# Performance work log

Measured on AMD Instinct MI355X. Metric: run time of the kernel, lower is better.

Reference implementation:

```python
import jax, jax.numpy as jnp
import numpy as np

N_NODES = 50000
N_EDGES = 800000
IN_DIM = 256
HID_DIM = 256
BATCH = 1


def setup_inputs() -> dict:
    key = jax.random.key(0)
    k1, k2, k3, k4, k5, k6, k7 = jax.random.split(key, 7)
    x = jax.random.normal(k1, (BATCH, N_NODES, IN_DIM), dtype=jnp.float32)
    edge_index = jax.random.randint(k2, (2, N_EDGES), 0, N_NODES, dtype=jnp.int32)
    # GCNConv params (glorot-ish scale)
    W1 = jax.random.normal(k3, (IN_DIM, HID_DIM), dtype=jnp.float32) * (1.0 / np.sqrt(IN_DIM))
    b1 = jnp.zeros((HID_DIM,), dtype=jnp.float32)
    W2 = jax.random.normal(k4, (HID_DIM, IN_DIM), dtype=jnp.float32) * (1.0 / np.sqrt(HID_DIM))
    b2 = jnp.zeros((IN_DIM,), dtype=jnp.float32)
    return {"x": x, "edge_index": edge_index, "W1": W1, "b1": b1, "W2": W2, "b2": b2}


def _gcn_conv(x, src, dst, norm, W, b):
    # x: [B, N, F_in] -> [B, N, F_out]; src/dst/norm: [E + N] (self-loops appended)
    h = x @ W                                   # linear transform first (PyG GCNConv)
    msg = h[:, src, :] * norm[None, :, None]    # gather + degree normalization
    out = jnp.zeros(h.shape, h.dtype).at[:, dst, :].add(msg)  # scatter-add
    return out + b


def _gcn_norm(edge_index, num_nodes):
    # symmetric normalization with self-loops: 1/sqrt(deg_i * deg_j)
    loop = jnp.arange(num_nodes, dtype=edge_index.dtype)
    src = jnp.concatenate([edge_index[0], loop])
    dst = jnp.concatenate([edge_index[1], loop])
    deg = jax.ops.segment_sum(jnp.ones(dst.shape, jnp.float32), dst, num_segments=num_nodes)
    dinv = jnp.where(deg > 0, jax.lax.rsqrt(jnp.maximum(deg, 1.0)), 0.0)
    norm = dinv[src] * dinv[dst]
    return src, dst, norm


def reference(x, edge_index, W1, b1, W2, b2):
    src, dst, norm = _gcn_norm(edge_index, x.shape[1])
    h = jax.nn.relu(_gcn_conv(x, src, dst, norm, W1, b1))
    h = jax.nn.relu(_gcn_conv(h, src, dst, norm, W2, b2))
    return (x + h) * 0.5
```

## Files before the change

kernel.cpp:

```cpp
#include <hip/hip_runtime.h>
#include <stdint.h>

#define NN 50000
#define NPAD 50048
#define NE 800000
#define DIM 256
#define NCHUNK 8
#define ZROW NN
#define GLC 64

typedef __attribute__((ext_vector_type(8))) short short8;
typedef __attribute__((ext_vector_type(4))) unsigned short ushort4v;
typedef __attribute__((ext_vector_type(8))) unsigned short ushort8v;
typedef __attribute__((ext_vector_type(4))) float floatx4;
typedef __attribute__((ext_vector_type(2))) float float2v;
typedef __attribute__((ext_vector_type(4))) uint32_t uint4v;
typedef __attribute__((ext_vector_type(4))) int int4v;

__device__ __forceinline__ uint16_t f2bf(float f) {
  union { float f; uint32_t u; } v; v.f = f;
  uint32_t r = v.u + 0x7fffu + ((v.u >> 16) & 1u);
  return (uint16_t)(r >> 16);
}
__device__ __forceinline__ float bf2f(uint16_t h) {
  union { uint32_t u; float f; } v; v.u = ((uint32_t)h) << 16;
  return v.f;
}

__device__ __forceinline__ void pkacc(float2v& a, uint32_t u) {
  union { uint32_t u; float f; } lo, hi;
  lo.u = u << 16;
  hi.u = u & 0xffff0000u;
  float2v val;
  val[0] = lo.f;
  val[1] = hi.f;
  asm("v_pk_add_f32 %0, %1, %0" : "+v"(a) : "v"(val));
}

__device__ __forceinline__ void stage16(const uint16_t* gp, short* lbase, int lane) {
#if __has_builtin(__builtin_amdgcn_global_load_lds)
  __builtin_amdgcn_global_load_lds((__attribute__((address_space(1))) void*)gp,
                                   (__attribute__((address_space(3))) void*)lbase,
                                   16, 0, 0);
#else
  *(ushort8v*)((uint16_t*)lbase + lane * 8) = *(const ushort8v*)gp;
#endif
}

__global__ __launch_bounds__(256) void k_init(int* __restrict__ fill, uint16_t* __restrict__ g,
                                              int* __restrict__ gl,
                                              const float* __restrict__ W1,
                                              const float* __restrict__ W2,
                                              uint16_t* __restrict__ Wt1,
                                              uint16_t* __restrict__ Wt2) {
  __shared__ float t[32][33];
  if (blockIdx.x >= 3125) {
    int bid = blockIdx.x - 3125;
    const float* W = (bid < 64) ? W1 : W2;
    uint16_t* Wt = (bid < 64) ? Wt1 : Wt2;
    bid &= 63;
    int bx = bid & 7, by = bid >> 3;
    int tx = threadIdx.x & 31, ty = threadIdx.x >> 5;
#pragma unroll
    for (int q = 0; q < 4; ++q)
      t[ty + q * 8][tx] = W[(size_t)(by * 32 + ty + q * 8) * 256 + bx * 32 + tx];
    __syncthreads();
#pragma unroll
    for (int q = 0; q < 4; ++q)
      Wt[(size_t)(bx * 32 + ty + q * 8) * 256 + by * 32 + tx] = f2bf(t[tx][ty + q * 8]);
    return;
  }
  int i4 = blockIdx.x * 256 + threadIdx.x;
  int4v z4 = {ZROW, ZROW, ZROW, ZROW};
  ((int4v*)gl)[i4] = z4;
  if (i4 < NPAD / 4) {
    int4v zz = {0, 0, 0, 0};
    ((int4v*)fill)[i4] = zz;
  }
  if (blockIdx.x < NCHUNK) {
    uint32_t* q = (uint32_t*)(g + ((size_t)blockIdx.x * NPAD + NN) * 32);
    for (int k = threadIdx.x; k < 768; k += 256) q[k] = 0;
  }
}

__global__ __launch_bounds__(256) void k_fill(const int* __restrict__ src,
                                              const int* __restrict__ dst,
                                              int* __restrict__ fill,
                                              int* __restrict__ gl) {
  int e = blockIdx.x * 256 + threadIdx.x;
  if (e < NE) {
    int d = dst[e];
    int old = atomicAdd(&fill[d], 1);
    if (old < GLC - 1) gl[d * GLC + old] = src[e];
  }
}

__global__ __launch_bounds__(256) void k_deg(const int* __restrict__ fill,
                                             int* __restrict__ gl) {
  int i = blockIdx.x * 256 + threadIdx.x;
  if (i < NN) {
    int deg = fill[i];
    if (deg < GLC) gl[i * GLC + deg] = i;
  }
}

#define BM 128
#define BK 32

template <int SPLIT>
__global__ __launch_bounds__(256) void k_gemm(const uint16_t* __restrict__ Ab,
                                              const float* __restrict__ Af,
                                              const uint16_t* __restrict__ Wt,
                                              const int* __restrict__ degp,
                                              uint16_t* __restrict__ C, int M) {
  __shared__ short Ash[2][BM * BK];
  __shared__ short Asl[2][BM * BK];
  __shared__ short Bs[2][128 * BK];

  const int tid = threadIdx.x;
  const int wave = tid >> 6, lane = tid & 63;
  const int wm = wave >> 1, wn = wave & 1;
  const int m16 = lane & 15, q = lane >> 4;
  const int rowBase = blockIdx.x * BM;
  const int colBase = blockIdx.y * 128;
  const int rsub = lane >> 2;
  const int kch = (lane & 3) * 8;

  auto stageB = [&](int kc, int buf) {
#pragma unroll
    for (int p2 = 0; p2 < 2; ++p2) {
      int n = p2 * 64 + wave * 16 + rsub;
      stage16(Wt + (size_t)(colBase + n) * 256 + kc * 32 + kch,
              &Bs[buf][(p2 * 64 + wave * 16) * BK], lane);
    }
  };
  auto stageA = [&](int kc, int buf) {
#pragma unroll
    for (int p2 = 0; p2 < 2; ++p2) {
      int r = rowBase + p2 * 64 + wave * 16 + rsub;
      stage16(Ab + ((size_t)kc * NPAD + r) * 32 + kch,
              &Ash[buf][(p2 * 64 + wave * 16) * BK], lane);
    }
  };
  auto loadA = [&](int kc, float4* f) {
#pragma unroll
    for (int p2 = 0; p2 < 2; ++p2) {
      int r = rowBase + p2 * 64 + wave * 16 + rsub;
      int rs = r < NN ? r : NN - 1;
      const float* xp = Af + (size_t)rs * DIM + kc * 32 + kch;
      f[2 * p2] = *(const float4*)xp;
      f[2 * p2 + 1] = *(const float4*)(xp + 4);
    }
  };
  auto writeA = [&](int buf, const float4* f) {
#pragma unroll
    for (int p2 = 0; p2 < 2; ++p2) {
      float ff[8] = {f[2 * p2].x, f[2 * p2].y, f[2 * p2].z, f[2 * p2].w,
                     f[2 * p2 + 1].x, f[2 * p2 + 1].y, f[2 * p2 + 1].z, f[2 * p2 + 1].w};
      short8 h8, l8;
#pragma unroll
      for (int u = 0; u < 8; ++u) {
        uint16_t hh = f2bf(ff[u]);
        h8[u] = (short)hh;
        l8[u] = (short)f2bf(ff[u] - bf2f(hh));
      }
      *(short8*)&Ash[buf][(p2 * 64 + wave * 16 + rsub) * BK + kch] = h8;
      *(short8*)&Asl[buf][(p2 * 64 + wave * 16 + rsub) * BK + kch] = l8;
    }
  };

  floatx4 acc[4][4];
#pragma unroll
  for (int i = 0; i < 4; ++i)
#pragma unroll
    for (int j = 0; j < 4; ++j) acc[i][j] = (floatx4)(0.0f);

  if (SPLIT) {
    float4 f[4];
    loadA(0, f);
    writeA(0, f);
  } else {
    stageA(0, 0);
  }
  stageB(0, 0);
  __syncthreads();

  for (int kc = 0; kc < 8; ++kc) {
    const int cur = kc & 1, nxt = cur ^ 1;
    float4 g4[4];
    if (kc < 7) {
      if (SPLIT) loadA(kc + 1, g4);
      else stageA(kc + 1, nxt);
      stageB(kc + 1, nxt);
    }

    short8 ah[4], al[4], b[4];
#pragma unroll
    for (int i = 0; i < 4; ++i) {
      int r = wm * 64 + i * 16 + m16;
      ah[i] = *(const short8*)(&Ash[cur][r * BK + q * 8]);
      if (SPLIT) al[i] = *(const short8*)(&Asl[cur][r * BK + q * 8]);
    }
#pragma unroll
    for (int j = 0; j < 4; ++j) {
      int n = wn * 64 + j * 16 + m16;
      b[j] = *(const short8*)(&Bs[cur][n * BK + q * 8]);
    }
#pragma unroll
    for (int i = 0; i < 4; ++i)
#pragma unroll
      for (int j = 0; j < 4; ++j) {
        if (SPLIT)
          acc[i][j] = __builtin_amdgcn_mfma_f32_16x16x32_bf16(al[i], b[j], acc[i][j], 0, 0, 0);
        acc[i][j] = __builtin_amdgcn_mfma_f32_16x16x32_bf16(ah[i], b[j], acc[i][j], 0, 0, 0);
      }

    if (SPLIT && kc < 7) writeA(nxt, g4);
    __syncthreads();
  }

#pragma unroll
  for (int i = 0; i < 4; ++i) {
#pragma unroll
    for (int reg = 0; reg < 4; ++reg) {
      int row = rowBase + wm * 64 + i * 16 + q * 4 + reg;
      if (row < M) {
        float dv = rsqrtf((float)(degp[row] + 1));
#pragma unroll
        for (int j = 0; j < 4; ++j) {
          int col = colBase + wn * 64 + j * 16 + m16;
          C[((size_t)(col >> 5) * NPAD + row) * 32 + (col & 31)] = f2bf(acc[i][j][reg] * dv);
        }
      }
    }
  }
}

template <int FINAL>
__global__ __launch_bounds__(256) void k_agg(const uint16_t* __restrict__ gb,
                                             const int* __restrict__ gl,
                                             const int* __restrict__ degp,
                                             const float* __restrict__ bias,
                                             const float* __restrict__ x,
                                             uint16_t* __restrict__ outb,
                                             float* __restrict__ outf) {
  const int c = blockIdx.x & 7;
  const int dg = blockIdx.x >> 3;
  const int wave = threadIdx.x >> 6, lane = threadIdx.x & 63;
  const int dl = lane >> 4;
  const int s = (lane >> 2) & 3;
  const int fl = lane & 3;
  const int d = dg * 16 + wave * 4 + dl;
  const uint16_t* gp = gb + (size_t)c * NPAD * 32;
  const uint32_t coff = (uint32_t)fl * 8;

  int ia[6];
#pragma unroll
  for (int j = 0; j < 6; ++j) ia[j] = gl[d * GLC + s + 4 * j];
  uint4v v[6];
#pragma unroll
  for (int j = 0; j < 6; ++j)
    v[j] = *(const uint4v*)(gp + (uint32_t)ia[j] * 32u + coff);

  float2v acc2[4];
#pragma unroll
  for (int j = 0; j < 4; ++j) acc2[j] = (float2v)(0.0f);
#pragma unroll
  for (int j = 0; j < 6; ++j) {
    pkacc(acc2[0], v[j][0]);
    pkacc(acc2[1], v[j][1]);
    pkacc(acc2[2], v[j][2]);
    pkacc(acc2[3], v[j][3]);
  }

  int deg = degp[d];
  if (deg >= 24) {
    for (int e = 24 + s; e <= deg; e += 4) {
      int si = gl[d * GLC + e];
      uint4v vt = *(const uint4v*)(gp + (uint32_t)si * 32u + coff);
      pkacc(acc2[0], vt[0]); pkacc(acc2[1], vt[1]);
      pkacc(acc2[2], vt[2]); pkacc(acc2[3], vt[3]);
    }
  }

#pragma unroll
  for (int j = 0; j < 4; ++j) {
    acc2[j][0] += __shfl_xor(acc2[j][0], 4);
    acc2[j][1] += __shfl_xor(acc2[j][1], 4);
    acc2[j][0] += __shfl_xor(acc2[j][0], 8);
    acc2[j][1] += __shfl_xor(acc2[j][1], 8);
  }

  if (s == 0) {
    float dd = rsqrtf((float)(deg + 1));
    int feat = c * 32 + fl * 8;
    float4 b0 = *(const float4*)(bias + feat);
    float4 b1 = *(const float4*)(bias + feat + 4);
    float bb[8] = {b0.x, b0.y, b0.z, b0.w, b1.x, b1.y, b1.z, b1.w};
    float r[8];
#pragma unroll
    for (int j = 0; j < 4; ++j) {
      r[2 * j] = fmaxf(dd * acc2[j][0] + bb[2 * j], 0.f);
      r[2 * j + 1] = fmaxf(dd * acc2[j][1] + bb[2 * j + 1], 0.f);
    }
    if (FINAL) {
      float4 x0 = *(const float4*)(x + (size_t)d * DIM + feat);
      float4 x1 = *(const float4*)(x + (size_t)d * DIM + feat + 4);
      float xx[8] = {x0.x, x0.y, x0.z, x0.w, x1.x, x1.y, x1.z, x1.w};
      float4 o0, o1;
      o0.x = (xx[0] + r[0]) * 0.5f; o0.y = (xx[1] + r[1]) * 0.5f;
      o0.z = (xx[2] + r[2]) * 0.5f; o0.w = (xx[3] + r[3]) * 0.5f;
      o1.x = (xx[4] + r[4]) * 0.5f; o1.y = (xx[5] + r[5]) * 0.5f;
      o1.z = (xx[6] + r[6]) * 0.5f; o1.w = (xx[7] + r[7]) * 0.5f;
      *(float4*)(outf + (size_t)d * DIM + feat) = o0;
      *(float4*)(outf + (size_t)d * DIM + feat + 4) = o1;
    } else {
      ushort8v o;
#pragma unroll
      for (int t = 0; t < 8; ++t) o[t] = f2bf(r[t]);
      *(ushort8v*)(outb + ((size_t)c * NPAD + d) * 32 + fl * 8) = o;
    }
  }
}

extern "C" void kernel_launch(void* const* d_in, const int* in_sizes, int n_in,
                              void* d_out, int out_size, void* d_ws, size_t ws_size,
                              hipStream_t stream) {
  const float* x  = (const float*)d_in[0];
  const int*   ei = (const int*)d_in[1];
  const float* W1 = (const float*)d_in[2];
  const float* b1 = (const float*)d_in[3];
  const float* W2 = (const float*)d_in[4];
  const float* b2 = (const float*)d_in[5];
  float* out = (float*)d_out;

  int*      fill   = (int*)d_ws;
  int*      gl     = fill + NPAD;
  uint16_t* Wt1    = (uint16_t*)(gl + NN * GLC);
  uint16_t* Wt2    = Wt1 + 256 * 256;
  uint16_t* g      = Wt2 + 256 * 256;
  uint16_t* h1     = g + (size_t)NPAD * DIM;

  const int* esrc = ei;
  const int* edst = ei + NE;

  k_init<<<3253, 256, 0, stream>>>(fill, g, gl, W1, W2, Wt1, Wt2);
  k_fill<<<(NE + 255) / 256, 256, 0, stream>>>(esrc, edst, fill, gl);
  k_deg<<<196, 256, 0, stream>>>(fill, gl);

  const int aggBlocks = NCHUNK * (NN / 16);
  dim3 ggrid(NPAD / BM, 2);
  k_gemm<1><<<ggrid, 256, 0, stream>>>(nullptr, x, Wt1, fill, g, NN);
  k_agg<0><<<aggBlocks, 256, 0, stream>>>(g, gl, fill, b1, nullptr, h1, nullptr);
  k_gemm<0><<<ggrid, 256, 0, stream>>>(h1, nullptr, Wt2, fill, g, NN);
  k_agg<1><<<aggBlocks, 256, 0, stream>>>(g, gl, fill, b2, x, nullptr, out);
}
```

Baseline: 288.0 us.

## Use 16-bit neighbor lists and degree-sorted node order in aggregation

```diff
diff --git a/kernel.cpp b/kernel.cpp
--- a/kernel.cpp
+++ b/kernel.cpp
@@ -10,7 +10,6 @@
 #define GLC 64
 
 typedef __attribute__((ext_vector_type(8))) short short8;
-typedef __attribute__((ext_vector_type(4))) unsigned short ushort4v;
 typedef __attribute__((ext_vector_type(8))) unsigned short ushort8v;
 typedef __attribute__((ext_vector_type(4))) float floatx4;
 typedef __attribute__((ext_vector_type(2))) float float2v;
@@ -48,14 +47,15 @@
 }
 
 __global__ __launch_bounds__(256) void k_init(int* __restrict__ fill, uint16_t* __restrict__ g,
-                                              int* __restrict__ gl,
+                                              uint16_t* __restrict__ gl,
+                                              int* __restrict__ bins,
                                               const float* __restrict__ W1,
                                               const float* __restrict__ W2,
                                               uint16_t* __restrict__ Wt1,
                                               uint16_t* __restrict__ Wt2) {
   __shared__ float t[32][33];
-  if (blockIdx.x >= 3125) {
-    int bid = blockIdx.x - 3125;
+  if (blockIdx.x >= 1563) {
+    int bid = blockIdx.x - 1563;
     const float* W = (bid < 64) ? W1 : W2;
     uint16_t* Wt = (bid < 64) ? Wt1 : Wt2;
     bid &= 63;
@@ -70,12 +70,18 @@
       Wt[(size_t)(bx * 32 + ty + q * 8) * 256 + by * 32 + tx] = f2bf(t[tx][ty + q * 8]);
     return;
   }
-  int i4 = blockIdx.x * 256 + threadIdx.x;
-  int4v z4 = {ZROW, ZROW, ZROW, ZROW};
-  ((int4v*)gl)[i4] = z4;
-  if (i4 < NPAD / 4) {
+  int i = blockIdx.x * 256 + threadIdx.x;
+  if (i < 400000) {
+    ushort8v z8 = {ZROW, ZROW, ZROW, ZROW, ZROW, ZROW, ZROW, ZROW};
+    ((ushort8v*)gl)[i] = z8;
+  }
+  if (i < NPAD / 4) {
     int4v zz = {0, 0, 0, 0};
-    ((int4v*)fill)[i4] = zz;
+    ((int4v*)fill)[i] = zz;
+  }
+  if (i < 32) {
+    int4v zz = {0, 0, 0, 0};
+    ((int4v*)bins)[i] = zz;
   }
   if (blockIdx.x < NCHUNK) {
     uint32_t* q = (uint32_t*)(g + ((size_t)blockIdx.x * NPAD + NN) * 32);
@@ -86,21 +92,41 @@
 __global__ __launch_bounds__(256) void k_fill(const int* __restrict__ src,
                                               const int* __restrict__ dst,
                                               int* __restrict__ fill,
-                                              int* __restrict__ gl) {
+                                              uint16_t* __restrict__ gl) {
   int e = blockIdx.x * 256 + threadIdx.x;
   if (e < NE) {
     int d = dst[e];
     int old = atomicAdd(&fill[d], 1);
-    if (old < GLC - 1) gl[d * GLC + old] = src[e];
-  }
-}
-
-__global__ __launch_bounds__(256) void k_deg(const int* __restrict__ fill,
-                                             int* __restrict__ gl) {
+    if (old < GLC - 1) gl[d * GLC + old] = (uint16_t)src[e];
+  }
+}
+
+__global__ __launch_bounds__(256) void k_degbins(const int* __restrict__ fill,
+                                                 uint16_t* __restrict__ gl,
+                                                 int* __restrict__ bins) {
   int i = blockIdx.x * 256 + threadIdx.x;
   if (i < NN) {
     int deg = fill[i];
-    if (deg < GLC) gl[i * GLC + deg] = i;
+    if (deg < GLC) gl[i * GLC + deg] = (uint16_t)i;
+    atomicAdd(&bins[deg < 63 ? deg : 63], 1);
+  }
+}
+
+__global__ __launch_bounds__(256) void k_scatter(const int* __restrict__ fill,
+                                                 int* __restrict__ bins,
+                                                 uint16_t* __restrict__ perm) {
+  __shared__ int soff[64];
+  if (threadIdx.x == 0) {
+    int a = 0;
+    for (int k = 0; k < 64; ++k) { soff[k] = a; a += bins[k]; }
+  }
+  __syncthreads();
+  int i = blockIdx.x * 256 + threadIdx.x;
+  if (i < NN) {
+    int deg = fill[i];
+    if (deg > 63) deg = 63;
+    int pos = soff[deg] + atomicAdd(&bins[64 + deg], 1);
+    perm[pos] = (uint16_t)i;
   }
 }
 
@@ -238,7 +264,8 @@
 
 template <int FINAL>
 __global__ __launch_bounds__(256) void k_agg(const uint16_t* __restrict__ gb,
-                                             const int* __restrict__ gl,
+                                             const uint16_t* __restrict__ perm,
+                                             const uint16_t* __restrict__ gl,
                                              const int* __restrict__ degp,
                                              const float* __restrict__ bias,
                                              const float* __restrict__ x,
@@ -250,36 +277,48 @@
   const int dl = lane >> 4;
   const int s = (lane >> 2) & 3;
   const int fl = lane & 3;
-  const int d = dg * 16 + wave * 4 + dl;
+  const int d = (int)perm[dg * 16 + wave * 4 + dl];
+  const int deg = degp[d];
   const uint16_t* gp = gb + (size_t)c * NPAD * 32;
   const uint32_t coff = (uint32_t)fl * 8;
-
-  int ia[6];
-#pragma unroll
-  for (int j = 0; j < 6; ++j) ia[j] = gl[d * GLC + s + 4 * j];
-  uint4v v[6];
-#pragma unroll
-  for (int j = 0; j < 6; ++j)
-    v[j] = *(const uint4v*)(gp + (uint32_t)ia[j] * 32u + coff);
+  const uint32_t* glr = (const uint32_t*)(gl + (size_t)d * GLC);
+
+  uint32_t w0 = glr[s], w1 = glr[s + 4], w2 = glr[s + 8];
+
+  auto gat = [&](uint32_t iu) -> uint4v {
+    return *(const uint4v*)(gp + iu * 32u + coff);
+  };
 
   float2v acc2[4];
 #pragma unroll
   for (int j = 0; j < 4; ++j) acc2[j] = (float2v)(0.0f);
-#pragma unroll
-  for (int j = 0; j < 6; ++j) {
-    pkacc(acc2[0], v[j][0]);
-    pkacc(acc2[1], v[j][1]);
-    pkacc(acc2[2], v[j][2]);
-    pkacc(acc2[3], v[j][3]);
-  }
-
-  int deg = degp[d];
+
+  uint4v v0 = gat(w0 & 0xffffu), v1 = gat(w0 >> 16);
+  uint4v v2 = gat(w1 & 0xffffu), v3 = gat(w1 >> 16);
+#pragma unroll
+  for (int j = 0; j < 4; ++j) {
+    pkacc(acc2[j], v0[j]);
+    pkacc(acc2[j], v1[j]);
+    pkacc(acc2[j], v2[j]);
+    pkacc(acc2[j], v3[j]);
+  }
+  if (deg >= 16) {
+    uint4v v4 = gat(w2 & 0xffffu), v5 = gat(w2 >> 16);
+#pragma unroll
+    for (int j = 0; j < 4; ++j) {
+      pkacc(acc2[j], v4[j]);
+      pkacc(acc2[j], v5[j]);
+    }
+  }
   if (deg >= 24) {
-    for (int e = 24 + s; e <= deg; e += 4) {
-      int si = gl[d * GLC + e];
-      uint4v vt = *(const uint4v*)(gp + (uint32_t)si * 32u + coff);
-      pkacc(acc2[0], vt[0]); pkacc(acc2[1], vt[1]);
-      pkacc(acc2[2], vt[2]); pkacc(acc2[3], vt[3]);
+    for (int k = 12 + s; 2 * k <= deg; k += 4) {
+      uint32_t w = glr[k];
+      uint4v va = gat(w & 0xffffu), vb = gat(w >> 16);
+#pragma unroll
+      for (int j = 0; j < 4; ++j) {
+        pkacc(acc2[j], va[j]);
+        pkacc(acc2[j], vb[j]);
+      }
     }
   }
 
@@ -335,8 +374,10 @@
   float* out = (float*)d_out;
 
   int*      fill   = (int*)d_ws;
-  int*      gl     = fill + NPAD;
-  uint16_t* Wt1    = (uint16_t*)(gl + NN * GLC);
+  int*      bins   = fill + NPAD;
+  uint16_t* perm   = (uint16_t*)(bins + 128);
+  uint16_t* gl     = perm + NN;
+  uint16_t* Wt1    = gl + (size_t)NN * GLC;
   uint16_t* Wt2    = Wt1 + 256 * 256;
   uint16_t* g      = Wt2 + 256 * 256;
   uint16_t* h1     = g + (size_t)NPAD * DIM;
@@ -344,14 +385,15 @@
   const int* esrc = ei;
   const int* edst = ei + NE;
 
-  k_init<<<3253, 256, 0, stream>>>(fill, g, gl, W1, W2, Wt1, Wt2);
+  k_init<<<1691, 256, 0, stream>>>(fill, g, gl, bins, W1, W2, Wt1, Wt2);
   k_fill<<<(NE + 255) / 256, 256, 0, stream>>>(esrc, edst, fill, gl);
-  k_deg<<<196, 256, 0, stream>>>(fill, gl);
+  k_degbins<<<196, 256, 0, stream>>>(fill, gl, bins);
+  k_scatter<<<196, 256, 0, stream>>>(fill, bins, perm);
 
   const int aggBlocks = NCHUNK * (NN / 16);
   dim3 ggrid(NPAD / BM, 2);
   k_gemm<1><<<ggrid, 256, 0, stream>>>(nullptr, x, Wt1, fill, g, NN);
-  k_agg<0><<<aggBlocks, 256, 0, stream>>>(g, gl, fill, b1, nullptr, h1, nullptr);
+  k_agg<0><<<aggBlocks, 256, 0, stream>>>(g, perm, gl, fill, b1, nullptr, h1, nullptr);
   k_gemm<0><<<ggrid, 256, 0, stream>>>(h1, nullptr, Wt2, fill, g, NN);
-  k_agg<1><<<aggBlocks, 256, 0, stream>>>(g, gl, fill, b2, x, nullptr, out);
-}
+  k_agg<1><<<aggBlocks, 256, 0, stream>>>(g, perm, gl, fill, b2, x, nullptr, out);
+}
```

Result: slower. 598.4 us (+107.8%).
